# Kernel optimization log

Hardware: AMD Instinct MI355X
Metric: run time of the kernel (lower is better)

## Reference

```python
import jax, jax.numpy as jnp
import numpy as np

C = 64
K = 16
DEPTH = 4            # int(sqrt(K))
N_NODES = K - 1      # 15 internal nodes per subspace tree
D = 512              # input feature dim, D // C = 8 per subspace
M = 512              # output dim (LUT rows)
N = 16384            # number of input rows


def _make_selection_matrix(C, depth=DEPTH):
    # row i within a subspace selects the transformed dim used at tree level of node i
    lvl = [0, 1, 1, 2, 2, 2, 2, 3, 3, 3, 3, 3, 3, 3, 3]
    S = np.zeros((C * N_NODES, C * depth), np.float32)
    for c in range(C):
        for i in range(N_NODES):
            S[c * N_NODES + i, c * depth + lvl[i]] = 1.0
    return S


def _make_bit_matrix(C, K=K):
    # per-subspace (K, K-1) matrix: leaf k gets +/-1 on the 4 nodes along its root-to-leaf path
    Bm = np.zeros((K, N_NODES), np.float32)
    for k in range(K):
        node = 0
        for l in range(DEPTH):
            bit = (k >> (DEPTH - 1 - l)) & 1
            Bm[k, node] = 1.0 if bit else -1.0
            node = 2 * node + 1 + bit  # children of node i are 2i+1 (left) and 2i+2 (right)
    Bfull = np.zeros((C * K, C * N_NODES), np.float32)
    for c in range(C):
        Bfull[c * K:(c + 1) * K, c * N_NODES:(c + 1) * N_NODES] = Bm
    return Bfull


def setup_inputs() -> dict:
    key = jax.random.key(0)
    k1, k2, k3, k4 = jax.random.split(key, 4)
    I = jax.random.normal(k1, (N, D), dtype=jnp.float32)
    A = jax.random.normal(k2, (C, D // C, DEPTH), dtype=jnp.float32) * (1.0 / np.sqrt(D // C))
    T = jax.random.normal(k3, (C * N_NODES,), dtype=jnp.float32) * 0.1
    L = jax.random.normal(k4, (M, C, K), dtype=jnp.float32)
    S = jnp.asarray(_make_selection_matrix(C))
    B = jnp.asarray(_make_bit_matrix(C))
    return {"I": I, "A": A, "T": T, "L": L, "S": S, "B": B}


def reference(I, A, T, L, S, B):
    C_, sub, depth = A.shape
    Kq = L.shape[-1]
    n = I.shape[0]
    # block-diagonal per-subspace projection: (n, D) -> (n, C*depth)
    Ir = I.T.reshape(C_, sub, n)                      # (C, sub, n)
    xt = jnp.einsum('csn,csd->cdn', Ir, A)            # (C, depth, n)
    xt = xt.reshape(C_ * depth, n)                    # (C*depth, n)
    # tree encoding: per-node activations, tanh relaxation, leaf scores
    h = S @ xt - T[:, None]                           # (C*15, n)
    b = (B @ jnp.tanh(h)).reshape(C_, Kq, n)          # (C, K, n)
    # straight-through hard one-hot encoding with softmax backward
    E_soft = jax.nn.softmax(b, axis=1)
    E_hard = jax.nn.one_hot(jnp.argmax(b, axis=1), Kq, axis=1, dtype=b.dtype)
    E = E_hard + E_soft - jax.lax.stop_gradient(E_soft)  # (C, K, n)
    # LUT decode: out[n, m] = sum_c L[m, c, enc(n, c)]
    out = jnp.einsum('mck,ckn->nm', L, E)
    return out
```

## Files before the change

kernel.cpp:

```cpp
#include <hip/hip_runtime.h>
#include <hip/hip_fp16.h>
#include <math.h>

#define CC 64
#define KK 16
#define NNODES 15
#define DD 512
#define MM 512
#define NN 16384

typedef _Float16 half8 __attribute__((ext_vector_type(8)));
typedef float f32x4 __attribute__((ext_vector_type(4)));
typedef unsigned long long u64;

__device__ __forceinline__ float xla_tanhf(float x) {
    const float kMax = 7.90531110763549805f;
    bool tiny = fabsf(x) < 0.0004f;
    float xc = fminf(fmaxf(x, -kMax), kMax);
    float x2 = __fmul_rn(xc, xc);
    float p = __fmaf_rn(x2, -2.76076847742355e-16f, 2.00018790482477e-13f);
    p = __fmaf_rn(x2, p, -8.60467152213735e-11f);
    p = __fmaf_rn(x2, p, 5.12229709037114e-08f);
    p = __fmaf_rn(x2, p, 1.48572235717979e-05f);
    p = __fmaf_rn(x2, p, 6.37261928875436e-04f);
    p = __fmaf_rn(x2, p, 4.89352455891786e-03f);
    p = __fmul_rn(xc, p);
    float q = __fmaf_rn(x2, 1.19825839466702e-06f, 1.18534705686654e-04f);
    q = __fmaf_rn(x2, q, 2.26843463243900e-03f);
    q = __fmaf_rn(x2, q, 4.89352518554385e-03f);
    return tiny ? x : __fdiv_rn(p, q);
}

__global__ __launch_bounds__(256) void pack_bfrag(const float* __restrict__ L,
                                                  uint4* __restrict__ Bpk) {
    const int t    = blockIdx.x * 256 + threadIdx.x;
    const int lane = t & 63;
    const int mtg  = (t >> 6) & 31;
    const int ks   = t >> 11;
    const int kbase = ks * 32 + ((lane >> 4) << 3);
    const int c     = kbase >> 4;
    const int slot0 = kbase & 15;
    const int m     = (mtg << 4) + (lane & 15);

    const float* src = L + ((size_t)m * CC + c) * KK + slot0;
    float4 v0 = ((const float4*)src)[0];
    float4 v1 = ((const float4*)src)[1];
    union { half8 h; uint4 u; } pk;
    pk.h[0] = (_Float16)v0.x; pk.h[1] = (_Float16)v0.y;
    pk.h[2] = (_Float16)v0.z; pk.h[3] = (_Float16)v0.w;
    pk.h[4] = (_Float16)v1.x; pk.h[5] = (_Float16)v1.y;
    pk.h[6] = (_Float16)v1.z; pk.h[7] = (_Float16)v1.w;
    Bpk[t] = pk.u;
}

__global__ __launch_bounds__(1024, 1) void fused_mfma(const float* __restrict__ I,
                                                      const float* __restrict__ A,
                                                      const float* __restrict__ T,
                                                      const uint4* __restrict__ Bpk,
                                                      float* __restrict__ out) {
    __shared__ float sA[32 * 64];
    __shared__ float sT[CC * NNODES];
    __shared__ unsigned sCodes[16 * 68];

    const int tid = threadIdx.x;
    for (int i = tid; i < CC * 32; i += 1024) sA[(i & 31) * 64 + (i >> 5)] = A[i];
    for (int i = tid; i < CC * NNODES; i += 1024) sT[i] = T[i];
    __syncthreads();

    const int w    = tid >> 6;
    const int lane = tid & 63;
    const int n0   = blockIdx.x * 64;

    {
        const int c = lane;
        const int lvl[NNODES] = {0, 1, 1, 2, 2, 2, 2, 3, 3, 3, 3, 3, 3, 3, 3};
        unsigned codeWord = 0;
#pragma unroll 2
        for (int rr = 0; rr < 4; ++rr) {
            const int rl = (rr << 4) + w;
            const float* Ij = I + (size_t)(n0 + rl) * DD + c * 8;
            float4 v0 = ((const float4*)Ij)[0];
            float4 v1 = ((const float4*)Ij)[1];
            float iv[8] = {v0.x, v0.y, v0.z, v0.w, v1.x, v1.y, v1.z, v1.w};

            float t[4] = {0.f, 0.f, 0.f, 0.f};
#pragma unroll
            for (int s = 0; s < 8; ++s) {
                float v = iv[s];
#pragma unroll
                for (int d = 0; d < 4; ++d)
                    t[d] = __fmaf_rn(v, sA[((s << 2) + d) * 64 + c], t[d]);
            }

            float th[NNODES];
#pragma unroll
            for (int i = 0; i < NNODES; ++i) {
                float h = __fsub_rn(t[lvl[i]], sT[c * NNODES + i]);
                th[i] = xla_tanhf(h);
            }

            int best = 0;
            float bestv = -3.0e38f;
#pragma unroll
            for (int k = 0; k < KK; ++k) {
                int node = 0;
                float s = 0.f;
#pragma unroll
                for (int l = 0; l < 4; ++l) {
                    int bit = (k >> (3 - l)) & 1;
                    s = __fadd_rn(s, bit ? th[node] : -th[node]);
                    node = 2 * node + 1 + bit;
                }
                if (s > bestv) { bestv = s; best = k; }
            }
            codeWord |= ((unsigned)best) << (rr << 3);
        }
        sCodes[w * 68 + c] = codeWord;
    }
    __syncthreads();

    const int wn   = w & 3;
    const int wm   = w >> 2;
    const int r15  = lane & 15;
    const int sb   = ((lane >> 4) & 1) << 3;
    const int chi  = lane >> 5;

    f32x4 acc[8];
#pragma unroll
    for (int mt = 0; mt < 8; ++mt) acc[mt] = (f32x4){0.f, 0.f, 0.f, 0.f};

    const uint4* Bp = Bpk + (size_t)(wm * 8) * 64 + lane;
    const unsigned* codeRow = sCodes + r15 * 68;
    const int wnsh = wn << 3;

    uint4 bX[8], bY[8];
#pragma unroll
    for (int mt = 0; mt < 8; ++mt) bX[mt] = Bp[mt * 64];
    unsigned cwA = codeRow[chi];
    unsigned cwB;

    for (int ks = 0; ks < 32; ks += 2) {
#pragma unroll
        for (int mt = 0; mt < 8; ++mt) bY[mt] = Bp[((ks + 1) * 32 + mt) * 64];
        cwB = codeRow[(ks + 1) * 2 + chi];

        {
            unsigned ud  = ((cwA >> wnsh) & 255u) - (unsigned)sb;
            unsigned ud2 = ud - 4u;
            u64 lo = (ud  < 4u) ? (0x3C00ull << ((ud  & 3u) << 4)) : 0ull;
            u64 hi = (ud2 < 4u) ? (0x3C00ull << ((ud2 & 3u) << 4)) : 0ull;
            union { u64 q[2]; half8 h; } uu; uu.q[0] = lo; uu.q[1] = hi;
#pragma unroll
            for (int mt = 0; mt < 8; ++mt) {
                union { uint4 u; half8 h; } bb; bb.u = bX[mt];
                acc[mt] = __builtin_amdgcn_mfma_f32_16x16x32_f16(uu.h, bb.h, acc[mt], 0, 0, 0);
            }
        }

        if (ks + 2 < 32) {
#pragma unroll
            for (int mt = 0; mt < 8; ++mt) bX[mt] = Bp[((ks + 2) * 32 + mt) * 64];
            cwA = codeRow[(ks + 2) * 2 + chi];
        }

        {
            unsigned ud  = ((cwB >> wnsh) & 255u) - (unsigned)sb;
            unsigned ud2 = ud - 4u;
            u64 lo = (ud  < 4u) ? (0x3C00ull << ((ud  & 3u) << 4)) : 0ull;
            u64 hi = (ud2 < 4u) ? (0x3C00ull << ((ud2 & 3u) << 4)) : 0ull;
            union { u64 q[2]; half8 h; } uu; uu.q[0] = lo; uu.q[1] = hi;
#pragma unroll
            for (int mt = 0; mt < 8; ++mt) {
                union { uint4 u; half8 h; } bb; bb.u = bY[mt];
                acc[mt] = __builtin_amdgcn_mfma_f32_16x16x32_f16(uu.h, bb.h, acc[mt], 0, 0, 0);
            }
        }
    }

    const int rbase = (lane >> 4) << 2;
#pragma unroll
    for (int mt = 0; mt < 8; ++mt) {
#pragma unroll
        for (int r = 0; r < 4; ++r) {
            out[(size_t)(n0 + (wn << 4) + rbase + r) * MM + (wm << 7) + (mt << 4) + r15] = acc[mt][r];
        }
    }
}

extern "C" void kernel_launch(void* const* d_in, const int* in_sizes, int n_in,
                              void* d_out, int out_size, void* d_ws, size_t ws_size,
                              hipStream_t stream) {
    const float* I = (const float*)d_in[0];
    const float* A = (const float*)d_in[1];
    const float* T = (const float*)d_in[2];
    const float* L = (const float*)d_in[3];

    uint4* Bpk = (uint4*)d_ws;
    float* out = (float*)d_out;

    hipLaunchKernelGGL(pack_bfrag, dim3(256), dim3(256), 0, stream, L, Bpk);
    hipLaunchKernelGGL(fused_mfma, dim3(NN / 64), dim3(1024), 0, stream, I, A, T, Bpk, out);
}
```

Measured before the change: 133.0 us.

## Split fused encode/decode kernel into separate encode and decode kernels

Splits the single 1024-thread fused kernel into an encode kernel that writes packed codes to a global workspace and a decode MFMA kernel that reads them, each using 256-thread blocks with four blocks per CU allowed. The encode kernel also keeps the A weights and thresholds in registers instead of re-reading LDS every row. The goal is more resident waves, so the latency-bound encode and the MFMA decode each get better occupancy and no longer stall on a shared block-wide barrier. The cost is an extra kernel launch and a round trip of the codes through global memory.

Measured after the change: 139.5 us. 4.9% more time.

```diff
diff --git a/kernel.cpp b/kernel.cpp
--- a/kernel.cpp
+++ b/kernel.cpp
@@ -53,85 +53,107 @@
     Bpk[t] = pk.u;
 }
 
-__global__ __launch_bounds__(1024, 1) void fused_mfma(const float* __restrict__ I,
-                                                      const float* __restrict__ A,
-                                                      const float* __restrict__ T,
-                                                      const uint4* __restrict__ Bpk,
-                                                      float* __restrict__ out) {
+__global__ __launch_bounds__(256, 4) void encode_kernel(const float* __restrict__ I,
+                                                        const float* __restrict__ A,
+                                                        const float* __restrict__ T,
+                                                        unsigned* __restrict__ codesG) {
     __shared__ float sA[32 * 64];
     __shared__ float sT[CC * NNODES];
+
+    const int tid = threadIdx.x;
+    for (int i = tid; i < CC * 32; i += 256) sA[(i & 31) * 64 + (i >> 5)] = A[i];
+    for (int i = tid; i < CC * NNODES; i += 256) sT[i] = T[i];
+    __syncthreads();
+
+    const int lane = tid & 63;
+    const int c    = lane;
+    const int w    = ((blockIdx.x & 3) << 2) + (tid >> 6);
+    const int tile = blockIdx.x >> 2;
+    const int n0   = tile * 64;
+
+    float a_[32];
+#pragma unroll
+    for (int i = 0; i < 32; ++i) a_[i] = sA[i * 64 + c];
+    float tt[NNODES];
+#pragma unroll
+    for (int i = 0; i < NNODES; ++i) tt[i] = sT[c * NNODES + i];
+
+    const int lvl[NNODES] = {0, 1, 1, 2, 2, 2, 2, 3, 3, 3, 3, 3, 3, 3, 3};
+    unsigned codeWord = 0;
+#pragma unroll 2
+    for (int rr = 0; rr < 4; ++rr) {
+        const int rl = (rr << 4) + w;
+        const float* Ij = I + (size_t)(n0 + rl) * DD + c * 8;
+        float4 v0 = ((const float4*)Ij)[0];
+        float4 v1 = ((const float4*)Ij)[1];
+        float iv[8] = {v0.x, v0.y, v0.z, v0.w, v1.x, v1.y, v1.z, v1.w};
+
+        float t[4] = {0.f, 0.f, 0.f, 0.f};
+#pragma unroll
+        for (int s = 0; s < 8; ++s) {
+            float v = iv[s];
+#pragma unroll
+            for (int d = 0; d < 4; ++d)
+                t[d] = __fmaf_rn(v, a_[(s << 2) + d], t[d]);
+        }
+
+        float th[NNODES];
+#pragma unroll
+        for (int i = 0; i < NNODES; ++i) {
+            float h = __fsub_rn(t[lvl[i]], tt[i]);
+            th[i] = xla_tanhf(h);
+        }
+
+        int best = 0;
+        float bestv = -3.0e38f;
+#pragma unroll
+        for (int k = 0; k < KK; ++k) {
+            int node = 0;
+            float s = 0.f;
+#pragma unroll
+            for (int l = 0; l < 4; ++l) {
+                int bit = (k >> (3 - l)) & 1;
+                s = __fadd_rn(s, bit ? th[node] : -th[node]);
+                node = 2 * node + 1 + bit;
+            }
+            if (s > bestv) { bestv = s; best = k; }
+        }
+        codeWord |= ((unsigned)best) << (rr << 3);
+    }
+    codesG[(size_t)tile * 1024 + (w << 6) + c] = codeWord;
+}
+
+__global__ __launch_bounds__(256, 4) void decode_kernel(const unsigned* __restrict__ codesG,
+                                                        const uint4* __restrict__ Bpk,
+                                                        float* __restrict__ out) {
     __shared__ unsigned sCodes[16 * 68];
 
-    const int tid = threadIdx.x;
-    for (int i = tid; i < CC * 32; i += 1024) sA[(i & 31) * 64 + (i >> 5)] = A[i];
-    for (int i = tid; i < CC * NNODES; i += 1024) sT[i] = T[i];
+    const int tid  = threadIdx.x;
+    const int tile = blockIdx.x >> 2;
+    const int mq   = blockIdx.x & 3;
+    const int n0   = tile * 64;
+
+#pragma unroll
+    for (int kk = 0; kk < 4; ++kk) {
+        int i = tid + (kk << 8);
+        sCodes[(i >> 6) * 68 + (i & 63)] = codesG[(size_t)tile * 1024 + i];
+    }
     __syncthreads();
 
     const int w    = tid >> 6;
     const int lane = tid & 63;
-    const int n0   = blockIdx.x * 64;
-
-    {
-        const int c = lane;
-        const int lvl[NNODES] = {0, 1, 1, 2, 2, 2, 2, 3, 3, 3, 3, 3, 3, 3, 3};
-        unsigned codeWord = 0;
-#pragma unroll 2
-        for (int rr = 0; rr < 4; ++rr) {
-            const int rl = (rr << 4) + w;
-            const float* Ij = I + (size_t)(n0 + rl) * DD + c * 8;
-            float4 v0 = ((const float4*)Ij)[0];
-            float4 v1 = ((const float4*)Ij)[1];
-            float iv[8] = {v0.x, v0.y, v0.z, v0.w, v1.x, v1.y, v1.z, v1.w};
-
-            float t[4] = {0.f, 0.f, 0.f, 0.f};
-#pragma unroll
-            for (int s = 0; s < 8; ++s) {
-                float v = iv[s];
-#pragma unroll
-                for (int d = 0; d < 4; ++d)
-                    t[d] = __fmaf_rn(v, sA[((s << 2) + d) * 64 + c], t[d]);
-            }
-
-            float th[NNODES];
-#pragma unroll
-            for (int i = 0; i < NNODES; ++i) {
-                float h = __fsub_rn(t[lvl[i]], sT[c * NNODES + i]);
-                th[i] = xla_tanhf(h);
-            }
-
-            int best = 0;
-            float bestv = -3.0e38f;
-#pragma unroll
-            for (int k = 0; k < KK; ++k) {
-                int node = 0;
-                float s = 0.f;
-#pragma unroll
-                for (int l = 0; l < 4; ++l) {
-                    int bit = (k >> (3 - l)) & 1;
-                    s = __fadd_rn(s, bit ? th[node] : -th[node]);
-                    node = 2 * node + 1 + bit;
-                }
-                if (s > bestv) { bestv = s; best = k; }
-            }
-            codeWord |= ((unsigned)best) << (rr << 3);
-        }
-        sCodes[w * 68 + c] = codeWord;
-    }
-    __syncthreads();
-
-    const int wn   = w & 3;
-    const int wm   = w >> 2;
+    const int wn   = w;
     const int r15  = lane & 15;
     const int sb   = ((lane >> 4) & 1) << 3;
     const int chi  = lane >> 5;
+    const int wnsh = wn << 3;
 
     f32x4 acc[8];
 #pragma unroll
     for (int mt = 0; mt < 8; ++mt) acc[mt] = (f32x4){0.f, 0.f, 0.f, 0.f};
 
-    const uint4* Bp = Bpk + (size_t)(wm * 8) * 64 + lane;
+    const uint4* Bp = Bpk + (size_t)(mq << 3) * 64 + lane;
     const unsigned* codeRow = sCodes + r15 * 68;
-    const int wnsh = wn << 3;
 
     uint4 bX[8], bY[8];
 #pragma unroll
@@ -182,7 +204,7 @@
     for (int mt = 0; mt < 8; ++mt) {
 #pragma unroll
         for (int r = 0; r < 4; ++r) {
-            out[(size_t)(n0 + (wn << 4) + rbase + r) * MM + (wm << 7) + (mt << 4) + r15] = acc[mt][r];
+            out[(size_t)(n0 + (wn << 4) + rbase + r) * MM + (mq << 7) + (mt << 4) + r15] = acc[mt][r];
         }
     }
 }
@@ -196,8 +218,10 @@
     const float* L = (const float*)d_in[3];
 
     uint4* Bpk = (uint4*)d_ws;
+    unsigned* codesG = (unsigned*)((char*)d_ws + (1 << 20));
     float* out = (float*)d_out;
 
     hipLaunchKernelGGL(pack_bfrag, dim3(256), dim3(256), 0, stream, L, Bpk);
-    hipLaunchKernelGGL(fused_mfma, dim3(NN / 64), dim3(1024), 0, stream, I, A, T, Bpk, out);
-}
+    hipLaunchKernelGGL(encode_kernel, dim3(1024), dim3(256), 0, stream, I, A, T, codesG);
+    hipLaunchKernelGGL(decode_kernel, dim3(1024), dim3(256), 0, stream, codesG, Bpk, out);
+}
```
